# Performance work log

Hardware: AMD Instinct MI355X
Metric: run time of the kernel (lower is better)

## Reference

```python
import jax, jax.numpy as jnp
import numpy as np

B = 8
N_NODES = 100000
N_EDGES = 800000
VOCAB = 50000
KGE = 128          # kge_size == gnn_hidden_size so all GAT layers share shapes
N_LAYERS = 3
HIDDEN = 1024
SEQ = 1024
DOWN = 256
T_PROMPT = 32
NEG_SLOPE = 0.2    # pyg GATConv default leaky_relu slope
COUNTS = np.array([11000, 12000, 12500, 12500, 13000, 12000, 13500, 13500])  # sums to N_NODES


def setup_inputs() -> dict:
    key = jax.random.key(0)
    ks = jax.random.split(key, 16)
    graph_x = jax.random.randint(ks[0], (N_NODES,), 0, VOCAB)
    edge_index = jax.random.randint(ks[1], (2, N_EDGES), 0, N_NODES)
    batch_ids = jnp.asarray(np.repeat(np.arange(B), COUNTS))  # sorted graph ids
    hidden_states = jax.random.normal(ks[2], (B, SEQ, HIDDEN), jnp.float32)
    seq_lengths = jax.random.randint(ks[3], (B,), 64, SEQ + 1)
    def glorot(k, shape, fan):
        return jax.random.normal(k, shape, jnp.float32) / np.sqrt(fan)
    return {
        "graph_x": graph_x,
        "edge_index": edge_index,
        "batch_ids": batch_ids,
        "hidden_states": hidden_states,
        "seq_lengths": seq_lengths,
        "emb_table": jax.random.normal(ks[4], (VOCAB, KGE), jnp.float32) * 0.02,
        "gat_W": glorot(ks[5], (N_LAYERS, KGE, KGE), KGE),
        "gat_asrc": glorot(ks[6], (N_LAYERS, KGE), KGE),
        "gat_adst": glorot(ks[7], (N_LAYERS, KGE), KGE),
        "gat_b": jnp.zeros((N_LAYERS, KGE), jnp.float32),
        "W_down": glorot(ks[8], (HIDDEN, DOWN), HIDDEN),
        "b_down": jnp.zeros((DOWN,), jnp.float32),
        "W_dc": glorot(ks[9], (KGE, DOWN), KGE),
        "b_dc": jnp.zeros((DOWN,), jnp.float32),
        "W_up": glorot(ks[10], (DOWN, HIDDEN), DOWN),
        "b_up": jnp.zeros((HIDDEN,), jnp.float32),
    }


def _gat_layer(x, W, a_s, a_d, b, src, dst, n):
    # pyg GATConv, heads=1: h = xW; e_ij = leaky_relu(a_s.h_j + a_d.h_i);
    # alpha = softmax over incoming edges of node i; out_i = sum_j alpha_ij h_j + b
    h = x @ W                                            # [N, F]
    e = jax.nn.leaky_relu((h @ a_s)[src] + (h @ a_d)[dst], NEG_SLOPE)  # [E]
    m = jax.ops.segment_max(e, dst, num_segments=n)
    ex = jnp.exp(e - m[dst])
    denom = jax.ops.segment_sum(ex, dst, num_segments=n)
    alpha = ex / denom[dst]
    out = jax.ops.segment_sum(alpha[:, None] * h[src], dst, num_segments=n)
    return out + b


def _adaptive_avg_pool(x, t):
    # torch AdaptiveAvgPool1d over length axis; x: [L, D], L static
    L = x.shape[0]
    cs = jnp.concatenate([jnp.zeros((1, x.shape[1]), x.dtype), jnp.cumsum(x, axis=0)], axis=0)
    idx = np.arange(t)
    starts = (idx * L) // t
    ends = -((-(idx + 1) * L) // t)  # ceil div
    return (cs[ends] - cs[starts]) / (ends - starts)[:, None].astype(x.dtype)


def reference(graph_x, edge_index, batch_ids, hidden_states, seq_lengths,
              emb_table, gat_W, gat_asrc, gat_adst, gat_b,
              W_down, b_down, W_dc, b_dc, W_up, b_up):
    n = graph_x.shape[0]
    self_loops = jnp.arange(n)
    src = jnp.concatenate([edge_index[0], self_loops])  # GATConv add_self_loops=True
    dst = jnp.concatenate([edge_index[1], self_loops])
    x = emb_table[graph_x]
    for l in range(N_LAYERS):
        x = _gat_layer(x, gat_W[l], gat_asrc[l], gat_adst[l], gat_b[l], src, dst, n)
        if l < N_LAYERS - 1:
            x = jax.nn.relu(x)  # basic_gnn default act between layers
    ctx = x @ W_dc + b_dc                                 # [N, DOWN]
    hs = hidden_states @ W_down + b_down                  # [B, S, DOWN]
    counts = np.bincount(np.asarray(batch_ids), minlength=B)
    offsets = np.concatenate([[0], np.cumsum(counts)])
    sl = np.asarray(seq_lengths)
    prompts = []
    for i in range(B):  # ragged per-example lengths (static at trace time)
        cat = jnp.concatenate([ctx[offsets[i]:offsets[i + 1]], hs[i, :sl[i]]], axis=0)
        prompts.append(_adaptive_avg_pool(cat, T_PROMPT))
    out = jax.nn.silu(jnp.stack(prompts, axis=0))         # [B, T, DOWN]
    return out @ W_up + b_up                              # dropout is identity in eval
```

## Files before the change

### kernel.cpp

```cpp
#include <hip/hip_runtime.h>
#include <hip/hip_bf16.h>

#define NN 100000
#define NE 800000
#define E2 900000
#define F  128
#define NB 8
#define SEQ 1024
#define HID 1024
#define DWN 256
#define TP 32

typedef __attribute__((ext_vector_type(4))) float f32x4;
typedef __attribute__((ext_vector_type(8))) short s16x8;

__device__ __forceinline__ float BL(uint u) { return __uint_as_float(u << 16); }
__device__ __forceinline__ float BH(uint u) { return __uint_as_float(u & 0xffff0000u); }
__device__ __forceinline__ uint PK(float lo, float hi) {
    __hip_bfloat16 a = __float2bfloat16(lo);
    __hip_bfloat16 b = __float2bfloat16(hi);
    return (uint)(*(ushort*)&a) | ((uint)(*(ushort*)&b) << 16);
}
__device__ __forceinline__ ushort B1(float v) {
    __hip_bfloat16 a = __float2bfloat16(v);
    return *(ushort*)&a;
}

__global__ void k_offsets(const int* __restrict__ bids, int* __restrict__ offs) {
    int n = blockIdx.x * 256 + threadIdx.x;
    if (n >= NN) return;
    int b = bids[n];
    if (n == 0) offs[0] = 0;
    else if (bids[n - 1] != b) offs[b] = n;
    if (n == NN - 1) offs[b + 1] = NN;
}

__global__ void k_embed(const int* __restrict__ gx, const float* __restrict__ emb,
                        ushort* __restrict__ x) {
    int i = blockIdx.x * 256 + threadIdx.x;
    int n = i >> 4, c = i & 15;
    const float4* src = (const float4*)(emb + (size_t)gx[n] * F + c * 8);
    float4 a = src[0], b = src[1];
    uint4 o;
    o.x = PK(a.x, a.y); o.y = PK(a.z, a.w);
    o.z = PK(b.x, b.y); o.w = PK(b.z, b.w);
    *(uint4*)&x[(size_t)n * F + c * 8] = o;
}

__global__ void k_wconv(const float* __restrict__ W, ushort* __restrict__ wt) {
    int l = blockIdx.x >> 7, col = blockIdx.x & 127, k = threadIdx.x;
    wt[l * 16384 + col * 128 + k] = B1(W[l * 16384 + k * 128 + col]);
}

__global__ void k_hist(const int* __restrict__ ei, int* __restrict__ counts) {
    int e = blockIdx.x * 256 + threadIdx.x;
    if (e >= E2) return;
    int dst = (e < NE) ? ei[NE + e] : (e - NE);
    atomicAdd(&counts[dst], 1);
}

__global__ void k_bsum(const int* __restrict__ counts, int* __restrict__ bsum) {
    __shared__ int red[256];
    int b = blockIdx.x, t = threadIdx.x;
    int base = b * 500;
    int s = 0;
    for (int i = t; i < 500; i += 256) s += counts[base + i];
    red[t] = s; __syncthreads();
    for (int o = 128; o > 0; o >>= 1) { if (t < o) red[t] += red[t + o]; __syncthreads(); }
    if (t == 0) bsum[b] = red[0];
}

__global__ void k_boff(const int* __restrict__ bsum, int* __restrict__ boff) {
    if (threadIdx.x == 0) {
        int r = 0;
        for (int i = 0; i < 200; i++) { boff[i] = r; r += bsum[i]; }
        boff[200] = r;
    }
}

__global__ __launch_bounds__(256) void k_scan(const int* __restrict__ counts,
                                              const int* __restrict__ boff,
                                              int* __restrict__ indptr,
                                              int* __restrict__ cursor) {
    __shared__ int sa[256], sb[256];
    int b = blockIdx.x, t = threadIdx.x;
    int base = b * 500;
    int i0 = t * 2, i1 = t * 2 + 1;
    int c0 = (i0 < 500) ? counts[base + i0] : 0;
    int c1 = (i1 < 500) ? counts[base + i1] : 0;
    sa[t] = c0 + c1;
    __syncthreads();
    int* src = sa; int* dst = sb;
    for (int off = 1; off < 256; off <<= 1) {
        int v = src[t];
        if (t >= off) v += src[t - off];
        dst[t] = v;
        __syncthreads();
        int* tmp = src; src = dst; dst = tmp;
    }
    int excl = src[t] - (c0 + c1) + boff[b];
    if (i0 < 500) { indptr[base + i0] = excl; cursor[base + i0] = excl; }
    if (i1 < 500) { indptr[base + i1] = excl + c0; cursor[base + i1] = excl + c0; }
    if (b == 199 && t == 0) indptr[NN] = E2;
}

__global__ void k_scatter(const int* __restrict__ ei, int* __restrict__ cursor,
                          int* __restrict__ srcs) {
    int e = blockIdx.x * 256 + threadIdx.x;
    if (e >= E2) return;
    int src, dst;
    if (e < NE) { src = ei[e]; dst = ei[NE + e]; }
    else        { src = dst = e - NE; }
    int pos = atomicAdd(&cursor[dst], 1);
    srcs[pos] = src;
}

__global__ __launch_bounds__(256) void k_gemm(
    const ushort* __restrict__ xb, const ushort* __restrict__ wt,
    const float* __restrict__ a_s, const float* __restrict__ a_d,
    ushort* __restrict__ hb, float* __restrict__ hs_src, float* __restrict__ hs_dst) {
    __shared__ uint4 As[128 * 16];
    __shared__ uint4 Bs[128 * 16];
    const int tid = threadIdx.x;
    const int wave = tid >> 6, lane = tid & 63;
    const int row0 = blockIdx.x * 128;
    const int lr = lane & 15, lg = lane >> 4;

    #pragma unroll
    for (int p = 0; p < 8; p++) {
        int id = p * 256 + tid;
        int row = id >> 4, c16 = id & 15;
        int rg = row0 + row; if (rg >= NN) rg = NN - 1;
        As[row * 16 + (c16 ^ (row & 7))] = *(const uint4*)&xb[(size_t)rg * F + c16 * 8];
        Bs[row * 16 + (c16 ^ (row & 7))] = *(const uint4*)&wt[row * F + c16 * 8];
    }
    __syncthreads();

    f32x4 acc[2][8];
    #pragma unroll
    for (int m = 0; m < 2; m++)
        #pragma unroll
        for (int n = 0; n < 8; n++) acc[m][n] = (f32x4){0.f, 0.f, 0.f, 0.f};

    #pragma unroll
    for (int kt = 0; kt < 4; kt++) {
        s16x8 a[2], b[8];
        #pragma unroll
        for (int m = 0; m < 2; m++) {
            int row = 32 * wave + 16 * m + lr;
            a[m] = *reinterpret_cast<const s16x8*>(&As[row * 16 + ((kt * 4 + lg) ^ (row & 7))]);
        }
        #pragma unroll
        for (int n = 0; n < 8; n++) {
            int col = 16 * n + lr;
            b[n] = *reinterpret_cast<const s16x8*>(&Bs[col * 16 + ((kt * 4 + lg) ^ (col & 7))]);
        }
        #pragma unroll
        for (int m = 0; m < 2; m++)
            #pragma unroll
            for (int n = 0; n < 8; n++)
                acc[m][n] = __builtin_amdgcn_mfma_f32_16x16x32_bf16(a[m], b[n], acc[m][n], 0, 0, 0);
    }

    float asv[8], adv[8];
    #pragma unroll
    for (int n = 0; n < 8; n++) { asv[n] = a_s[16 * n + lr]; adv[n] = a_d[16 * n + lr]; }

    #pragma unroll
    for (int m = 0; m < 2; m++) {
        #pragma unroll
        for (int r = 0; r < 4; r++) {
            int rg = row0 + 32 * wave + 16 * m + lg * 4 + r;
            bool ok = rg < NN;
            float ps = 0.f, pd = 0.f;
            #pragma unroll
            for (int n = 0; n < 8; n++) {
                float v = acc[m][n][r];
                if (ok) hb[(size_t)rg * F + 16 * n + lr] = B1(v);
                ps += v * asv[n]; pd += v * adv[n];
            }
            #pragma unroll
            for (int msk = 8; msk >= 1; msk >>= 1) {
                ps += __shfl_xor(ps, msk);
                pd += __shfl_xor(pd, msk);
            }
            if (ok && lr == 0) { hs_src[rg] = ps; hs_dst[rg] = pd; }
        }
    }
}

__global__ __launch_bounds__(256) void k_agg(
    const ushort* __restrict__ hb, const int* __restrict__ srcs,
    const int* __restrict__ indptr, const float* __restrict__ hs_src,
    const float* __restrict__ hs_dst, const float* __restrict__ bias,
    ushort* __restrict__ xout, int do_relu) {
    __shared__ uint2 se[4][64];
    int wave = threadIdx.x >> 6, lane = threadIdx.x & 63;
    int i = blockIdx.x * 4 + wave;
    if (i >= NN) return;
    int p0 = indptr[i], p1 = indptr[i + 1];
    int deg = p1 - p0;
    float hd = hs_dst[i];
    float ax0 = 0.f, ay0 = 0.f, ax1 = 0.f, ay1 = 0.f;
    float ax2 = 0.f, ay2 = 0.f, ax3 = 0.f, ay3 = 0.f, dl = 0.f;

    if (deg <= 64) {
        int s = 0; float e = -1e30f;
        if (lane < deg) {
            s = srcs[p0 + lane];
            float t0 = hs_src[s] + hd;
            e = t0 > 0.f ? t0 : 0.2f * t0;
        }
        float m = e;
        #pragma unroll
        for (int o = 32; o > 0; o >>= 1) m = fmaxf(m, __shfl_xor(m, o));
        float ex = (lane < deg) ? __expf(e - m) : 0.f;
        dl = ex;
        se[wave][lane] = make_uint2((unsigned)s, __float_as_uint(ex));
        int j = 0;
        for (; j + 4 <= deg; j += 4) {
            uint2 q0 = se[wave][j + 0], q1 = se[wave][j + 1];
            uint2 q2 = se[wave][j + 2], q3 = se[wave][j + 3];
            uint h0 = ((const uint*)(hb + (size_t)q0.x * F))[lane];
            uint h1 = ((const uint*)(hb + (size_t)q1.x * F))[lane];
            uint h2 = ((const uint*)(hb + (size_t)q2.x * F))[lane];
            uint h3 = ((const uint*)(hb + (size_t)q3.x * F))[lane];
            float e0 = __uint_as_float(q0.y), e1 = __uint_as_float(q1.y);
            float e2 = __uint_as_float(q2.y), e3 = __uint_as_float(q3.y);
            ax0 += e0 * BL(h0); ay0 += e0 * BH(h0);
            ax1 += e1 * BL(h1); ay1 += e1 * BH(h1);
            ax2 += e2 * BL(h2); ay2 += e2 * BH(h2);
            ax3 += e3 * BL(h3); ay3 += e3 * BH(h3);
        }
        for (; j < deg; j++) {
            uint2 q = se[wave][j];
            uint h = ((const uint*)(hb + (size_t)q.x * F))[lane];
            float e0 = __uint_as_float(q.y);
            ax0 += e0 * BL(h); ay0 += e0 * BH(h);
        }
    } else {
        float m = -1e30f;
        for (int p = p0 + lane; p < p1; p += 64) {
            int s = srcs[p];
            float e = hs_src[s] + hd;
            e = e > 0.f ? e : 0.2f * e;
            m = fmaxf(m, e);
        }
        #pragma unroll
        for (int o = 32; o > 0; o >>= 1) m = fmaxf(m, __shfl_xor(m, o));
        for (int base = p0; base < p1; base += 64) {
            int cn = min(64, p1 - base);
            int s = 0; float ex = 0.f;
            if (lane < cn) {
                s = srcs[base + lane];
                float e = hs_src[s] + hd;
                e = e > 0.f ? e : 0.2f * e;
                ex = __expf(e - m);
            }
            dl += ex;
            se[wave][lane] = make_uint2((unsigned)s, __float_as_uint(ex));
            int j = 0;
            for (; j + 4 <= cn; j += 4) {
                uint2 q0 = se[wave][j + 0], q1 = se[wave][j + 1];
                uint2 q2 = se[wave][j + 2], q3 = se[wave][j + 3];
                uint h0 = ((const uint*)(hb + (size_t)q0.x * F))[lane];
                uint h1 = ((const uint*)(hb + (size_t)q1.x * F))[lane];
                uint h2 = ((const uint*)(hb + (size_t)q2.x * F))[lane];
                uint h3 = ((const uint*)(hb + (size_t)q3.x * F))[lane];
                float e0 = __uint_as_float(q0.y), e1 = __uint_as_float(q1.y);
                float e2 = __uint_as_float(q2.y), e3 = __uint_as_float(q3.y);
                ax0 += e0 * BL(h0); ay0 += e0 * BH(h0);
                ax1 += e1 * BL(h1); ay1 += e1 * BH(h1);
                ax2 += e2 * BL(h2); ay2 += e2 * BH(h2);
                ax3 += e3 * BL(h3); ay3 += e3 * BH(h3);
            }
            for (; j < cn; j++) {
                uint2 q = se[wave][j];
                uint h = ((const uint*)(hb + (size_t)q.x * F))[lane];
                float e0 = __uint_as_float(q.y);
                ax0 += e0 * BL(h); ay0 += e0 * BH(h);
            }
        }
    }
    float accx = (ax0 + ax1) + (ax2 + ax3);
    float accy = (ay0 + ay1) + (ay2 + ay3);
    #pragma unroll
    for (int o = 32; o > 0; o >>= 1) dl += __shfl_xor(dl, o);
    float inv = 1.f / dl;
    float2 b2 = ((const float2*)bias)[lane];
    float ox = accx * inv + b2.x;
    float oy = accy * inv + b2.y;
    if (do_relu) { ox = fmaxf(ox, 0.f); oy = fmaxf(oy, 0.f); }
    ((uint*)xout)[(size_t)i * 64 + lane] = PK(ox, oy);
}

__global__ __launch_bounds__(256) void k_binsum_ctx(
    const ushort* __restrict__ x3, const int* __restrict__ bids,
    const int* __restrict__ offs, const int* __restrict__ seq_len,
    float* __restrict__ s128) {
    int wid = blockIdx.x * 4 + (threadIdx.x >> 6);
    int lane = threadIdx.x & 63;
    int r0 = wid * 64;
    if (r0 >= NN) return;
    int r1 = min(r0 + 64, NN);
    float ax = 0.f, ay = 0.f;
    int cur = -1;
    int cb = -1, off = 0, C = 0, L = 1;
    for (int r = r0; r < r1; r++) {
        int b = bids[r];
        if (b != cb) { cb = b; off = offs[b]; C = offs[b + 1] - off; L = C + seq_len[b]; }
        int q = r - off;
        int tmin = (q * TP) / L;
        int tmax = ((q + 1) * TP - 1) / L;
        uint v = ((const uint*)(x3 + (size_t)r * F))[lane];
        float vx = BL(v), vy = BH(v);
        int bin = b * TP + tmin;
        if (bin != cur) {
            if (cur >= 0) {
                atomicAdd(&s128[(size_t)cur * F + 2 * lane], ax);
                atomicAdd(&s128[(size_t)cur * F + 2 * lane + 1], ay);
            }
            cur = bin; ax = 0.f; ay = 0.f;
        }
        ax += vx; ay += vy;
        if (tmax != tmin) {
            atomicAdd(&s128[(size_t)(b * TP + tmax) * F + 2 * lane], vx);
            atomicAdd(&s128[(size_t)(b * TP + tmax) * F + 2 * lane + 1], vy);
        }
    }
    if (cur >= 0) {
        atomicAdd(&s128[(size_t)cur * F + 2 * lane], ax);
        atomicAdd(&s128[(size_t)cur * F + 2 * lane + 1], ay);
    }
}

__global__ __launch_bounds__(256) void k_binsum_hid(
    const float* __restrict__ hidden, const int* __restrict__ offs,
    const int* __restrict__ seq_len, float* __restrict__ s1024) {
    int wid = blockIdx.x * 4 + (threadIdx.x >> 6);
    int lane = threadIdx.x & 63;
    int b = wid >> 7;
    int chunk = wid & 127;
    int sl = seq_len[b];
    int r0 = chunk * 8;
    if (r0 >= sl) return;
    int r1 = min(r0 + 8, sl);
    int C = offs[b + 1] - offs[b];
    int L = C + sl;
    float a[16];
    #pragma unroll
    for (int c = 0; c < 16; c++) a[c] = 0.f;
    int cur = -1;
    const float* hbase = hidden + (size_t)b * SEQ * HID;
    for (int r = r0; r < r1; r++) {
        int q = C + r;
        int tmin = (q * TP) / L;
        int tmax = ((q + 1) * TP - 1) / L;
        const float4* row = (const float4*)(hbase + (size_t)r * HID);
        float4 v0 = row[lane], v1 = row[64 + lane], v2 = row[128 + lane], v3 = row[192 + lane];
        int bin = b * TP + tmin;
        if (bin != cur) {
            if (cur >= 0) {
                float* dst = s1024 + (size_t)cur * HID;
                #pragma unroll
                for (int c = 0; c < 4; c++) atomicAdd(&dst[4 * lane + c], a[c]);
                #pragma unroll
                for (int c = 0; c < 4; c++) atomicAdd(&dst[256 + 4 * lane + c], a[4 + c]);
                #pragma unroll
                for (int c = 0; c < 4; c++) atomicAdd(&dst[512 + 4 * lane + c], a[8 + c]);
                #pragma unroll
                for (int c = 0; c < 4; c++) atomicAdd(&dst[768 + 4 * lane + c], a[12 + c]);
            }
            cur = bin;
            #pragma unroll
            for (int c = 0; c < 16; c++) a[c] = 0.f;
        }
        a[0] += v0.x; a[1] += v0.y; a[2] += v0.z; a[3] += v0.w;
        a[4] += v1.x; a[5] += v1.y; a[6] += v1.z; a[7] += v1.w;
        a[8] += v2.x; a[9] += v2.y; a[10] += v2.z; a[11] += v2.w;
        a[12] += v3.x; a[13] += v3.y; a[14] += v3.z; a[15] += v3.w;
        if (tmax != tmin) {
            float* dst = s1024 + (size_t)(b * TP + tmax) * HID;
            atomicAdd(&dst[4 * lane + 0], v0.x); atomicAdd(&dst[4 * lane + 1], v0.y);
            atomicAdd(&dst[4 * lane + 2], v0.z); atomicAdd(&dst[4 * lane + 3], v0.w);
            atomicAdd(&dst[256 + 4 * lane + 0], v1.x); atomicAdd(&dst[256 + 4 * lane + 1], v1.y);
            atomicAdd(&dst[256 + 4 * lane + 2], v1.z); atomicAdd(&dst[256 + 4 * lane + 3], v1.w);
            atomicAdd(&dst[512 + 4 * lane + 0], v2.x); atomicAdd(&dst[512 + 4 * lane + 1], v2.y);
            atomicAdd(&dst[512 + 4 * lane + 2], v2.z); atomicAdd(&dst[512 + 4 * lane + 3], v2.w);
            atomicAdd(&dst[768 + 4 * lane + 0], v3.x); atomicAdd(&dst[768 + 4 * lane + 1], v3.y);
            atomicAdd(&dst[768 + 4 * lane + 2], v3.z); atomicAdd(&dst[768 + 4 * lane + 3], v3.w);
        }
    }
    if (cur >= 0) {
        float* dst = s1024 + (size_t)cur * HID;
        #pragma unroll
        for (int c = 0; c < 4; c++) atomicAdd(&dst[4 * lane + c], a[c]);
        #pragma unroll
        for (int c = 0; c < 4; c++) atomicAdd(&dst[256 + 4 * lane + c], a[4 + c]);
        #pragma unroll
        for (int c = 0; c < 4; c++) atomicAdd(&dst[512 + 4 * lane + c], a[8 + c]);
        #pragma unroll
        for (int c = 0; c < 4; c++) atomicAdd(&dst[768 + 4 * lane + c], a[12 + c]);
    }
}

__global__ __launch_bounds__(1024) void k_sp(
    const float* __restrict__ s128, const float* __restrict__ s1024,
    const int* __restrict__ offs, const int* __restrict__ seq_len,
    const float* __restrict__ W_dc, const float* __restrict__ b_dc,
    const float* __restrict__ W_down, const float* __restrict__ b_down,
    float* __restrict__ sp) {
    __shared__ float red[4][DWN];
    int bin = blockIdx.x;
    int b = bin >> 5, t = bin & 31;
    int c = threadIdx.x & 255, ks = threadIdx.x >> 8;
    int C = offs[b + 1] - offs[b];
    int sl = seq_len[b];
    int L = C + sl;
    int start = (t * L) / TP;
    int end = ((t + 1) * L + TP - 1) / TP;
    int cnt = end - start;
    int ce = min(end, C);
    int n_ctx = max(ce - start, 0);
    int n_hs = max(end - C, 0) - max(start - C, 0);
    float p = 0.f;
    int k0 = ks * 288, k1 = k0 + 288;
    for (int k = k0; k < k1; k++) {
        if (k < F) p += s128[(size_t)bin * F + k] * W_dc[k * DWN + c];
        else {
            int kk = k - F;
            p += s1024[(size_t)bin * HID + kk] * W_down[kk * DWN + c];
        }
    }
    red[ks][c] = p;
    __syncthreads();
    if (ks == 0) {
        p = (red[0][c] + red[1][c]) + (red[2][c] + red[3][c])
            + (float)n_ctx * b_dc[c] + (float)n_hs * b_down[c];
        p /= (float)cnt;
        sp[(size_t)bin * DWN + c] = p / (1.f + __expf(-p));
    }
}

__global__ __launch_bounds__(256) void k_up(
    const float* __restrict__ sp, const float* __restrict__ W_up,
    const float* __restrict__ b_up, float* __restrict__ out) {
    __shared__ float s[DWN];
    int bin = blockIdx.x >> 2, q = blockIdx.x & 3;
    int tid = threadIdx.x;
    s[tid] = sp[(size_t)bin * DWN + tid];
    __syncthreads();
    int o = q * 256 + tid;
    float a0 = 0.f, a1 = 0.f, a2 = 0.f, a3 = 0.f;
    #pragma unroll 4
    for (int k = 0; k < DWN; k += 4) {
        a0 += s[k + 0] * W_up[(size_t)(k + 0) * HID + o];
        a1 += s[k + 1] * W_up[(size_t)(k + 1) * HID + o];
        a2 += s[k + 2] * W_up[(size_t)(k + 2) * HID + o];
        a3 += s[k + 3] * W_up[(size_t)(k + 3) * HID + o];
    }
    out[(size_t)bin * HID + o] = (a0 + a1) + (a2 + a3) + b_up[o];
}

extern "C" void kernel_launch(void* const* d_in, const int* in_sizes, int n_in,
                              void* d_out, int out_size, void* d_ws, size_t ws_size,
                              hipStream_t stream) {
    const int*   graph_x   = (const int*)d_in[0];
    const int*   edge_idx  = (const int*)d_in[1];
    const int*   batch_ids = (const int*)d_in[2];
    const float* hidden    = (const float*)d_in[3];
    const int*   seq_len   = (const int*)d_in[4];
    const float* emb       = (const float*)d_in[5];
    const float* gat_W     = (const float*)d_in[6];
    const float* gat_as    = (const float*)d_in[7];
    const float* gat_ad    = (const float*)d_in[8];
    const float* gat_b     = (const float*)d_in[9];
    const float* W_down    = (const float*)d_in[10];
    const float* b_down    = (const float*)d_in[11];
    const float* W_dc      = (const float*)d_in[12];
    const float* b_dc      = (const float*)d_in[13];
    const float* W_up      = (const float*)d_in[14];
    const float* b_up      = (const float*)d_in[15];
    float* out = (float*)d_out;

    char* ws = (char*)d_ws;
    ushort* bufA   = (ushort*)(ws);
    ushort* Wt     = (ushort*)(ws + 26000000);
    ushort* hb     = (ushort*)(ws + 51200000);
    float*  s128   = (float*) (ws + 80000000);
    float*  s1024  = (float*) (ws + 80131072);
    float*  sp     = (float*) (ws + 81179648);
    float*  hs_src = (float*) (ws + 102400000);
    float*  hs_dst = (float*) (ws + 102800000);
    int*    counts = (int*)   (ws + 103200000);
    int*    indptr = (int*)   (ws + 103600000);
    int*    cursor = (int*)   (ws + 104000128);
    int*    srcs   = (int*)   (ws + 104400128);
    int*    bsum   = (int*)   (ws + 108000128);
    int*    boff   = (int*)   (ws + 108001128);
    int*    offs   = (int*)   (ws + 108002128);

    hipMemsetAsync(counts, 0, NN * sizeof(int), stream);
    k_offsets<<<(NN + 255) / 256, 256, 0, stream>>>(batch_ids, offs);
    k_embed<<<NN * 16 / 256, 256, 0, stream>>>(graph_x, emb, bufA);
    k_wconv<<<384, 128, 0, stream>>>(gat_W, Wt);
    k_hist<<<(E2 + 255) / 256, 256, 0, stream>>>(edge_idx, counts);
    k_bsum<<<200, 256, 0, stream>>>(counts, bsum);
    k_boff<<<1, 64, 0, stream>>>(bsum, boff);
    k_scan<<<200, 256, 0, stream>>>(counts, boff, indptr, cursor);
    k_scatter<<<(E2 + 255) / 256, 256, 0, stream>>>(edge_idx, cursor, srcs);

    for (int l = 0; l < 3; l++) {
        k_gemm<<<(NN + 127) / 128, 256, 0, stream>>>(bufA, Wt + l * F * F, gat_as + l * F,
                                                     gat_ad + l * F, hb, hs_src, hs_dst);
        k_agg<<<(NN + 3) / 4, 256, 0, stream>>>(hb, srcs, indptr, hs_src, hs_dst,
                                                gat_b + l * F, bufA, (l < 2) ? 1 : 0);
    }

    hipMemsetAsync((void*)s128, 0, 131072 + 1048576, stream);
    k_binsum_ctx<<<391, 256, 0, stream>>>(bufA, batch_ids, offs, seq_len, s128);
    k_binsum_hid<<<256, 256, 0, stream>>>(hidden, offs, seq_len, s1024);
    k_sp<<<NB * TP, 1024, 0, stream>>>(s128, s1024, offs, seq_len,
                                       W_dc, b_dc, W_down, b_down, sp);
    k_up<<<NB * TP * 4, 256, 0, stream>>>(sp, W_up, b_up, out);
}
```

Measured before the change: 422.1 us.

## Build CSR via coarse dst-bucketing and per-bucket LDS counting sort

Replaces the five-kernel CSR construction (global histogram, block sums, offsets, scan, atomic scatter) with three steps. Edges are first binned into 256-node buckets in a fixed-capacity staging buffer, each packed as src<<8 | local dst. A single-thread pass computes the bucket offsets, then one block per bucket counting-sorts its edges in shared memory and writes indptr and srcs contiguously. This cuts kernel launches and the per-node global atomics and scattered writes. The cost is heavy atomic contention on only 392 bucket counters, and correctness depends on no bucket exceeding 4096 edges.

```diff
diff --git a/kernel.cpp b/kernel.cpp
--- a/kernel.cpp
+++ b/kernel.cpp
@@ -10,6 +10,8 @@
 #define HID 1024
 #define DWN 256
 #define TP 32
+#define NBK 392
+#define BCAP 4096
 
 typedef __attribute__((ext_vector_type(4))) float f32x4;
 typedef __attribute__((ext_vector_type(8))) short s16x8;
@@ -52,67 +54,69 @@
     wt[l * 16384 + col * 128 + k] = B1(W[l * 16384 + k * 128 + col]);
 }
 
-__global__ void k_hist(const int* __restrict__ ei, int* __restrict__ counts) {
-    int e = blockIdx.x * 256 + threadIdx.x;
-    if (e >= E2) return;
-    int dst = (e < NE) ? ei[NE + e] : (e - NE);
-    atomicAdd(&counts[dst], 1);
-}
-
-__global__ void k_bsum(const int* __restrict__ counts, int* __restrict__ bsum) {
-    __shared__ int red[256];
-    int b = blockIdx.x, t = threadIdx.x;
-    int base = b * 500;
-    int s = 0;
-    for (int i = t; i < 500; i += 256) s += counts[base + i];
-    red[t] = s; __syncthreads();
-    for (int o = 128; o > 0; o >>= 1) { if (t < o) red[t] += red[t + o]; __syncthreads(); }
-    if (t == 0) bsum[b] = red[0];
-}
-
-__global__ void k_boff(const int* __restrict__ bsum, int* __restrict__ boff) {
-    if (threadIdx.x == 0) {
-        int r = 0;
-        for (int i = 0; i < 200; i++) { boff[i] = r; r += bsum[i]; }
-        boff[200] = r;
-    }
-}
-
-__global__ __launch_bounds__(256) void k_scan(const int* __restrict__ counts,
-                                              const int* __restrict__ boff,
-                                              int* __restrict__ indptr,
-                                              int* __restrict__ cursor) {
-    __shared__ int sa[256], sb[256];
-    int b = blockIdx.x, t = threadIdx.x;
-    int base = b * 500;
-    int i0 = t * 2, i1 = t * 2 + 1;
-    int c0 = (i0 < 500) ? counts[base + i0] : 0;
-    int c1 = (i1 < 500) ? counts[base + i1] : 0;
-    sa[t] = c0 + c1;
-    __syncthreads();
-    int* src = sa; int* dst = sb;
-    for (int off = 1; off < 256; off <<= 1) {
-        int v = src[t];
-        if (t >= off) v += src[t - off];
-        dst[t] = v;
-        __syncthreads();
-        int* tmp = src; src = dst; dst = tmp;
-    }
-    int excl = src[t] - (c0 + c1) + boff[b];
-    if (i0 < 500) { indptr[base + i0] = excl; cursor[base + i0] = excl; }
-    if (i1 < 500) { indptr[base + i1] = excl + c0; cursor[base + i1] = excl + c0; }
-    if (b == 199 && t == 0) indptr[NN] = E2;
-}
-
-__global__ void k_scatter(const int* __restrict__ ei, int* __restrict__ cursor,
-                          int* __restrict__ srcs) {
+__global__ void k_bucket(const int* __restrict__ ei, int* __restrict__ bcur,
+                         uint* __restrict__ stage) {
     int e = blockIdx.x * 256 + threadIdx.x;
     if (e >= E2) return;
     int src, dst;
     if (e < NE) { src = ei[e]; dst = ei[NE + e]; }
     else        { src = dst = e - NE; }
-    int pos = atomicAdd(&cursor[dst], 1);
-    srcs[pos] = src;
+    int g = dst >> 8;
+    int pos = atomicAdd(&bcur[g], 1);
+    stage[(size_t)g * BCAP + pos] = ((uint)src << 8) | (uint)(dst & 255);
+}
+
+__global__ void k_boff(const int* __restrict__ bcur, int* __restrict__ boff,
+                       int* __restrict__ indptr) {
+    if (threadIdx.x == 0) {
+        int r = 0;
+        for (int i = 0; i < NBK; i++) { boff[i] = r; r += bcur[i]; }
+        boff[NBK] = r;
+        indptr[NN] = E2;
+    }
+}
+
+__global__ __launch_bounds__(256) void k_sort(
+    const uint* __restrict__ stage, const int* __restrict__ bcur,
+    const int* __restrict__ boff, int* __restrict__ indptr,
+    int* __restrict__ srcs) {
+    __shared__ int lcur[256];
+    __shared__ int sa[256], sb[256];
+    __shared__ uint sorted[BCAP];
+    int g = blockIdx.x, t = threadIdx.x;
+    int ecnt = bcur[g];
+    int base = boff[g];
+    const uint* slab = stage + (size_t)g * BCAP;
+    lcur[t] = 0;
+    __syncthreads();
+    for (int i = t; i < ecnt; i += 256)
+        atomicAdd(&lcur[slab[i] & 255u], 1);
+    __syncthreads();
+    int myc = lcur[t];
+    sa[t] = myc;
+    __syncthreads();
+    int* s = sa; int* d = sb;
+    for (int off = 1; off < 256; off <<= 1) {
+        int v = s[t];
+        if (t >= off) v += s[t - off];
+        d[t] = v;
+        __syncthreads();
+        int* tmp = s; s = d; d = tmp;
+    }
+    int excl = s[t] - myc;
+    int node = g * 256 + t;
+    if (node < NN) indptr[node] = base + excl;
+    __syncthreads();
+    lcur[t] = excl;
+    __syncthreads();
+    for (int i = t; i < ecnt; i += 256) {
+        uint p = slab[i];
+        int pos = atomicAdd(&lcur[p & 255u], 1);
+        sorted[pos] = p >> 8;
+    }
+    __syncthreads();
+    for (int i = t; i < ecnt; i += 256)
+        srcs[base + i] = (int)sorted[i];
 }
 
 __global__ __launch_bounds__(256) void k_gemm(
@@ -490,25 +494,22 @@
     float*  s128   = (float*) (ws + 80000000);
     float*  s1024  = (float*) (ws + 80131072);
     float*  sp     = (float*) (ws + 81179648);
+    uint*   stage  = (uint*)  (ws + 82000000);
     float*  hs_src = (float*) (ws + 102400000);
     float*  hs_dst = (float*) (ws + 102800000);
-    int*    counts = (int*)   (ws + 103200000);
+    int*    bcur   = (int*)   (ws + 103200000);
+    int*    boff   = (int*)   (ws + 103210000);
     int*    indptr = (int*)   (ws + 103600000);
-    int*    cursor = (int*)   (ws + 104000128);
     int*    srcs   = (int*)   (ws + 104400128);
-    int*    bsum   = (int*)   (ws + 108000128);
-    int*    boff   = (int*)   (ws + 108001128);
     int*    offs   = (int*)   (ws + 108002128);
 
-    hipMemsetAsync(counts, 0, NN * sizeof(int), stream);
+    hipMemsetAsync(bcur, 0, NBK * sizeof(int), stream);
     k_offsets<<<(NN + 255) / 256, 256, 0, stream>>>(batch_ids, offs);
     k_embed<<<NN * 16 / 256, 256, 0, stream>>>(graph_x, emb, bufA);
     k_wconv<<<384, 128, 0, stream>>>(gat_W, Wt);
-    k_hist<<<(E2 + 255) / 256, 256, 0, stream>>>(edge_idx, counts);
-    k_bsum<<<200, 256, 0, stream>>>(counts, bsum);
-    k_boff<<<1, 64, 0, stream>>>(bsum, boff);
-    k_scan<<<200, 256, 0, stream>>>(counts, boff, indptr, cursor);
-    k_scatter<<<(E2 + 255) / 256, 256, 0, stream>>>(edge_idx, cursor, srcs);
+    k_bucket<<<(E2 + 255) / 256, 256, 0, stream>>>(edge_idx, bcur, stage);
+    k_boff<<<1, 64, 0, stream>>>(bcur, boff, indptr);
+    k_sort<<<NBK, 256, 0, stream>>>(stage, bcur, boff, indptr, srcs);
 
     for (int l = 0; l < 3; l++) {
         k_gemm<<<(NN + 127) / 128, 256, 0, stream>>>(bufA, Wt + l * F * F, gat_as + l * F,
```

After: 731.7 us. +73.3%, slower.
